# Performance work log

Hardware: AMD Instinct MI355X
Metric: run time of the kernel (lower is better)

The kernel has to match this reference:

```python
import jax, jax.numpy as jnp
import numpy as np

N_NODES = 50000
N_EDGES = 800000
F_IN = 32
H = 128
N_REL = 4
MAX_DEG = 10
N_GRAPHS = 64
N_BLOCKS = 2


def setup_inputs() -> dict:
    key = jax.random.key(0)
    ks = jax.random.split(key, 20)
    s = 0.05
    return {
        "x": jax.random.normal(ks[0], (N_NODES, F_IN), jnp.float32),
        "edge_index": jax.random.randint(ks[1], (2, N_EDGES), 0, N_NODES, dtype=jnp.int32),
        "edge_attr": jax.random.randint(ks[2], (N_EDGES,), 0, N_REL, dtype=jnp.int32),
        "batch_idx": jnp.sort(jax.random.randint(ks[3], (N_NODES,), 0, N_GRAPHS, dtype=jnp.int32)),
        "embed_W": jax.random.normal(ks[4], (F_IN, H), jnp.float32) * s,
        "embed_b": jax.random.normal(ks[5], (H,), jnp.float32) * s,
        "rgcn_Wrel": jax.random.normal(ks[6], (N_BLOCKS, N_REL, H, H), jnp.float32) * s,
        "rgcn_Wroot": jax.random.normal(ks[7], (N_BLOCKS, H, H), jnp.float32) * s,
        "rgcn_b": jax.random.normal(ks[8], (N_BLOCKS, H), jnp.float32) * s,
        "mf_Wl": jax.random.normal(ks[9], (N_BLOCKS, MAX_DEG + 1, H, H), jnp.float32) * s,
        "mf_bl": jax.random.normal(ks[10], (N_BLOCKS, MAX_DEG + 1, H), jnp.float32) * s,
        "mf_Wr": jax.random.normal(ks[11], (N_BLOCKS, MAX_DEG + 1, H, H), jnp.float32) * s,
        "lin1_W": jax.random.normal(ks[12], (H, H), jnp.float32) * s,
        "lin1_b": jax.random.normal(ks[13], (H,), jnp.float32) * s,
        "lin2_W": jax.random.normal(ks[14], (H, 1), jnp.float32) * s,
        "lin2_b": jax.random.normal(ks[15], (1,), jnp.float32) * s,
    }


def _rgcn(x, src, dst, rel, Wrel, Wroot, b):
    # PyG RGCNConv with default aggr='mean': per-relation mean over incoming
    # edges, then per-relation weight, plus root transform and bias.
    seg = dst * N_REL + rel  # composite segment id: (node, relation)
    agg = jax.ops.segment_sum(x[src], seg, num_segments=N_NODES * N_REL)
    cnt = jax.ops.segment_sum(jnp.ones((seg.shape[0],), x.dtype), seg,
                              num_segments=N_NODES * N_REL)
    agg = (agg / jnp.maximum(cnt, 1.0)[:, None]).reshape(N_NODES, N_REL, H)
    return jnp.einsum('nrh,rho->no', agg, Wrel) + x @ Wroot + b


def _mfconv(x, src, dst, Wl, bl, Wr):
    # PyG MFConv: sum-aggregate neighbors, then per-degree-bucket linear heads
    # (degree = in-degree clamped to MAX_DEG); lin_r applied to root x (no bias).
    h = jax.ops.segment_sum(x[src], dst, num_segments=N_NODES)  # [N,H]
    deg = jax.ops.segment_sum(jnp.ones((src.shape[0],), jnp.int32), dst,
                              num_segments=N_NODES)
    deg = jnp.minimum(deg, MAX_DEG)  # [N]
    # out_all: [D+1, N, H] candidate outputs, one per degree bucket
    out_all = (jnp.einsum('nh,dho->dno', h, Wl)
               + jnp.einsum('nh,dho->dno', x, Wr)
               + bl[:, None, :])
    return jnp.take_along_axis(out_all, deg[None, :, None], axis=0)[0]


def reference(x, edge_index, edge_attr, batch_idx, embed_W, embed_b,
              rgcn_Wrel, rgcn_Wroot, rgcn_b, mf_Wl, mf_bl, mf_Wr,
              lin1_W, lin1_b, lin2_W, lin2_b):
    src, dst = edge_index[0], edge_index[1]
    h = x @ embed_W + embed_b
    for blk in range(N_BLOCKS):
        if blk > 0:  # first block uses Identity instead of ReLU
            h = jax.nn.relu(h)
        h = _rgcn(h, src, dst, edge_attr, rgcn_Wrel[blk], rgcn_Wroot[blk], rgcn_b[blk])
        h = jax.nn.relu(h)
        h = _mfconv(h, src, dst, mf_Wl[blk], mf_bl[blk], mf_Wr[blk])
    g = jax.ops.segment_sum(h, batch_idx, num_segments=N_GRAPHS)  # global_add_pool
    g = jax.nn.relu(g @ lin1_W + lin1_b)
    return g @ lin2_W + lin2_b
```

## Files before the change

### kernel.cpp

```cpp
#include <hip/hip_runtime.h>
#include <hip/hip_bf16.h>

#define NRELS 4
#define MAXDEG 10
#define NBUCK 11
#define POOL_CHUNKS 8

typedef __attribute__((ext_vector_type(8))) short s16x8;
typedef __attribute__((ext_vector_type(4))) float f32x4;
typedef __attribute__((ext_vector_type(8))) unsigned short u16x8;

__device__ inline unsigned short f2b(float f) {
  __hip_bfloat16 h = __float2bfloat16(f);
  return *reinterpret_cast<unsigned short*>(&h);
}
__device__ inline float b2f(unsigned short u) {
  union { unsigned int i; float f; } v;
  v.i = ((unsigned int)u) << 16;
  return v.f;
}
__device__ inline float blo(unsigned int v) {
  union { unsigned int i; float f; } x;
  x.i = v << 16;
  return x.f;
}
__device__ inline float bhi(unsigned int v) {
  union { unsigned int i; float f; } x;
  x.i = v & 0xffff0000u;
  return x.f;
}

typedef __attribute__((address_space(3))) unsigned int lds_uint;
typedef __attribute__((address_space(1))) const unsigned int glob_uint;
__device__ __forceinline__ void gld_lds16(const void* g, void* l) {
  __builtin_amdgcn_global_load_lds((glob_uint*)g, (lds_uint*)l, 16, 0, 0);
}

__global__ __launch_bounds__(512) void coarse_count_scan(
    const int* __restrict__ dst, int* __restrict__ bhist, int* __restrict__ boff,
    int* __restrict__ bcur, int* __restrict__ done, int* __restrict__ perm, int permCap,
    int NB, int E, int nblocks) {
  __shared__ int lh[512];
  __shared__ int lastf;
  int t = threadIdx.x;
  lh[t] = 0;
  __syncthreads();
  for (int i = blockIdx.x * 512 + t; i < permCap; i += nblocks * 512) perm[i] = -1;
  int base = blockIdx.x * 4096;
  int lim = E - base;
  if (lim > 4096) lim = 4096;
  for (int i = t; i < lim; i += 512) atomicAdd(&lh[dst[base + i] >> 7], 1);
  __syncthreads();
  if (lh[t]) atomicAdd(&bhist[t], lh[t]);
  __threadfence();
  __syncthreads();
  if (t == 0) lastf = (atomicAdd(done, 1) == nblocks - 1) ? 1 : 0;
  __syncthreads();
  if (!lastf) return;
  int v = (t < NB) ? atomicAdd(&bhist[t], 0) : 0;
  lh[t] = v;
  __syncthreads();
  for (int o = 1; o < 512; o <<= 1) {
    int x = (t >= o) ? lh[t - o] : 0;
    __syncthreads();
    lh[t] += x;
    __syncthreads();
  }
  if (t < NB) {
    int st = lh[t] - v;
    boff[t] = st;
    bcur[t] = st;
  }
  if (t == 0) boff[NB] = E;
}

__global__ __launch_bounds__(512) void coarse_scatter(
    const int* __restrict__ src, const int* __restrict__ dst, const int* __restrict__ rel,
    int* __restrict__ bcur, uint2* __restrict__ ebuf, int E) {
  __shared__ int lhist[512];
  __shared__ int lstart[512];
  __shared__ int lcur[512];
  __shared__ int gbase[512];
  __shared__ uint2 stage[4096];
  int t = threadIdx.x;
  lhist[t] = 0;
  __syncthreads();
  int base = blockIdx.x * 4096;
  int lim = E - base;
  if (lim > 4096) lim = 4096;
  for (int i = t; i < lim; i += 512) atomicAdd(&lhist[dst[base + i] >> 7], 1);
  __syncthreads();
  int myc = lhist[t];
  lstart[t] = myc;
  __syncthreads();
  for (int o = 1; o < 512; o <<= 1) {
    int x = (t >= o) ? lstart[t - o] : 0;
    __syncthreads();
    lstart[t] += x;
    __syncthreads();
  }
  int incl = lstart[t];
  __syncthreads();
  lstart[t] = incl - myc;
  lcur[t] = 0;
  if (myc > 0) gbase[t] = atomicAdd(&bcur[t], myc);
  __syncthreads();
  for (int i = t; i < lim; i += 512) {
    int e = base + i;
    int d = dst[e];
    int b = d >> 7;
    int slot = lstart[b] + atomicAdd(&lcur[b], 1);
    stage[slot] = make_uint2((unsigned)(d * 4 + rel[e]), (unsigned)src[e]);
  }
  __syncthreads();
  for (int i = t; i < lim; i += 512) {
    uint2 val = stage[i];
    int b = (int)(val.x >> 9);
    ebuf[gbase[b] + (i - lstart[b])] = val;
  }
}

__global__ __launch_bounds__(512) void fine_place(
    const uint2* __restrict__ ebuf, const int* __restrict__ boff, int* __restrict__ cnt,
    int* __restrict__ seg_start, float* __restrict__ inv, int* __restrict__ deg,
    int* __restrict__ bucket, int* __restrict__ hist, int* __restrict__ csr, int NSEG) {
  __shared__ int lh[512];
  __shared__ int sc[512];
  __shared__ int lcur[512];
  __shared__ int lbh[16];
  int t = threadIdx.x;
  int b = blockIdx.x;
  lh[t] = 0;
  if (t < 16) lbh[t] = 0;
  __syncthreads();
  int s = boff[b], e = boff[b + 1];
  for (int i = s + t; i < e; i += 512) atomicAdd(&lh[ebuf[i].x & 511], 1);
  __syncthreads();
  int v = lh[t];
  sc[t] = v;
  __syncthreads();
  for (int o = 1; o < 512; o <<= 1) {
    int x = (t >= o) ? sc[t - o] : 0;
    __syncthreads();
    sc[t] += x;
    __syncthreads();
  }
  int gseg = b * 512 + t;
  int mystart = s + sc[t] - v;
  lcur[t] = mystart;
  if (gseg < NSEG) {
    cnt[gseg] = v;
    seg_start[gseg] = mystart;
    inv[gseg] = 1.0f / (float)(v > 1 ? v : 1);
    if ((t & 3) == 0) {
      int d = sc[t + 3] - sc[t] + v;
      int n = gseg >> 2;
      deg[n] = d;
      int bk = d < MAXDEG ? d : MAXDEG;
      bucket[n] = bk;
      atomicAdd(&lbh[bk], 1);
    }
  }
  __syncthreads();
  if (t < NBUCK && lbh[t]) atomicAdd(&hist[t], lbh[t]);
  for (int i = s + t; i < e; i += 512) {
    uint2 vv = ebuf[i];
    int pos = atomicAdd(&lcur[vv.x & 511], 1);
    csr[pos] = (int)vv.y;
  }
}

__global__ void build_perm(const int* __restrict__ bucket, const int* __restrict__ hist,
                           int* __restrict__ fill, int* __restrict__ perm, int N) {
  __shared__ int soff[NBUCK];
  __shared__ int lh[NBUCK];
  __shared__ int gbase[NBUCK];
  int t = threadIdx.x;
  if (t < NBUCK) lh[t] = 0;
  if (t == 0) {
    int acc = 0;
    for (int b = 0; b < NBUCK; b++) {
      soff[b] = acc;
      acc += ((hist[b] + 63) >> 6) << 6;
    }
  }
  __syncthreads();
  int n = blockIdx.x * 256 + t;
  int b = -1, lr = 0;
  if (n < N) {
    b = bucket[n];
    lr = atomicAdd(&lh[b], 1);
  }
  __syncthreads();
  if (t < NBUCK && lh[t] > 0) gbase[t] = atomicAdd(&fill[t * 16], lh[t]);
  __syncthreads();
  if (n < N) perm[soff[b] + gbase[b] + lr] = n;
}

__global__ __launch_bounds__(256) void embed_conv(
    const float* __restrict__ x, const float* __restrict__ embW,
    const float* __restrict__ bias, const float* __restrict__ Wrel,
    const float* __restrict__ Wroot, const float* __restrict__ Wl,
    const float* __restrict__ Wr, unsigned short* __restrict__ Bt,
    unsigned short* __restrict__ Btm, unsigned short* __restrict__ out, int N, int nbE) {
  if ((int)blockIdx.x >= nbE) {
    const int R1 = 2 * 128 * 640;
    const int R2 = R1 + 2 * 11 * 128 * 256;
    int t = (blockIdx.x - nbE) * 256 + threadIdx.x;
    if (t < R1) {
      int blk = t / 81920;
      int rem = t % 81920;
      int n = rem / 640;
      int k = rem % 640;
      float v;
      if (k < 512)
        v = Wrel[(size_t)blk * 65536 + (size_t)k * 128 + n];
      else
        v = Wroot[(size_t)blk * 16384 + (size_t)(k - 512) * 128 + n];
      Bt[t] = f2b(v);
    } else if (t < R2) {
      int t2 = t - R1;
      int k = t2 & 255;
      int n = (t2 >> 8) & 127;
      int bb = (t2 >> 15) % 11;
      int blk = t2 / (11 * 128 * 256);
      float v;
      if (k < 128)
        v = Wl[(((size_t)blk * 11 + bb) * 128 + k) * 128 + n];
      else
        v = Wr[(((size_t)blk * 11 + bb) * 128 + (k - 128)) * 128 + n];
      Btm[t2] = f2b(v);
    }
    return;
  }
  __shared__ unsigned char As[64 * 80];
  __shared__ unsigned char Bs[128 * 80];
  int t = threadIdx.x;
  int m0 = blockIdx.x * 64;
  {
    int r = t >> 2, s = t & 3;
    int gr = m0 + r;
    if (gr >= N) gr = N - 1;
    const float* xp = x + (size_t)gr * 32 + s * 8;
    float4 f0 = *(const float4*)xp;
    float4 f1 = *(const float4*)(xp + 4);
    u16x8 o;
    o[0] = f2b(f0.x); o[1] = f2b(f0.y); o[2] = f2b(f0.z); o[3] = f2b(f0.w);
    o[4] = f2b(f1.x); o[5] = f2b(f1.y); o[6] = f2b(f1.z); o[7] = f2b(f1.w);
    *(u16x8*)(As + r * 80 + s * 16) = o;
  }
  {
    int n = t >> 1, hf = t & 1;
    unsigned short tmp[16];
#pragma unroll
    for (int j = 0; j < 16; j++) tmp[j] = f2b(embW[(size_t)(hf * 16 + j) * 128 + n]);
    *(u16x8*)(Bs + n * 80 + hf * 32) = *(u16x8*)tmp;
    *(u16x8*)(Bs + n * 80 + hf * 32 + 16) = *(u16x8*)(tmp + 8);
  }
  __syncthreads();
  int lane = t & 63, wave = t >> 6;
  int row = lane & 15, quad = lane >> 4;
  int nh = wave * 32;
  f32x4 acc[2][4];
#pragma unroll
  for (int i = 0; i < 2; i++)
#pragma unroll
    for (int j = 0; j < 4; j++) acc[i][j] = (f32x4){0.f, 0.f, 0.f, 0.f};
  s16x8 af[4], bf[2];
#pragma unroll
  for (int mt = 0; mt < 4; mt++) {
    int R = mt * 16 + row;
    af[mt] = *(const s16x8*)(As + R * 80 + quad * 16);
  }
#pragma unroll
  for (int nt = 0; nt < 2; nt++) {
    int R = nh + nt * 16 + row;
    bf[nt] = *(const s16x8*)(Bs + R * 80 + quad * 16);
  }
#pragma unroll
  for (int nt = 0; nt < 2; nt++)
#pragma unroll
    for (int mt = 0; mt < 4; mt++)
      acc[nt][mt] = __builtin_amdgcn_mfma_f32_16x16x32_bf16(af[mt], bf[nt], acc[nt][mt], 0, 0, 0);
#pragma unroll
  for (int nt = 0; nt < 2; nt++) {
    int n = nh + nt * 16 + row;
    float bv = bias[n];
#pragma unroll
    for (int mt = 0; mt < 4; mt++) {
#pragma unroll
      for (int r4 = 0; r4 < 4; r4++) {
        int m = m0 + mt * 16 + quad * 4 + r4;
        if (m < N) out[(size_t)m * 128 + n] = f2b(acc[nt][mt][r4] + bv);
      }
    }
  }
}

__device__ __forceinline__ void acc8v(float* a, uint4 v) {
  a[0] += blo(v.x); a[1] += bhi(v.x);
  a[2] += blo(v.y); a[3] += bhi(v.y);
  a[4] += blo(v.z); a[5] += bhi(v.z);
  a[6] += blo(v.w); a[7] += bhi(v.w);
}

__device__ __forceinline__ void gather_seg(const unsigned short* __restrict__ hb,
                                           const int* __restrict__ csr, int st, int cn,
                                           int chunk, float* a) {
  const unsigned short* hq = hb + chunk * 16;
  int i = 0;
  for (; i + 2 <= cn; i += 2) {
    int p0 = csr[st + i], p1 = csr[st + i + 1];
    const uint4* r0 = (const uint4*)(hq + (size_t)p0 * 128);
    const uint4* r1 = (const uint4*)(hq + (size_t)p1 * 128);
    uint4 v00 = r0[0], v01 = r0[1];
    uint4 v10 = r1[0], v11 = r1[1];
    acc8v(a + 0, v00); acc8v(a + 8, v01);
    acc8v(a + 0, v10); acc8v(a + 8, v11);
  }
  if (i < cn) {
    const uint4* r0 = (const uint4*)(hq + (size_t)csr[st + i] * 128);
    acc8v(a + 0, r0[0]); acc8v(a + 8, r0[1]);
  }
}

__device__ __forceinline__ void gather2_seg(const unsigned short* __restrict__ hb,
                                            const int* __restrict__ csr,
                                            int st0, int cn0, int st1, int cn1,
                                            int chunk, float* a0, float* a1) {
  const unsigned short* hq = hb + chunk * 16;
  int mn = cn0 < cn1 ? cn0 : cn1;
  int i = 0;
  for (; i + 2 <= mn; i += 2) {
    int p00 = csr[st0 + i], p01 = csr[st0 + i + 1];
    int p10 = csr[st1 + i], p11 = csr[st1 + i + 1];
    const uint4* r00 = (const uint4*)(hq + (size_t)p00 * 128);
    const uint4* r01 = (const uint4*)(hq + (size_t)p01 * 128);
    const uint4* r10 = (const uint4*)(hq + (size_t)p10 * 128);
    const uint4* r11 = (const uint4*)(hq + (size_t)p11 * 128);
    uint4 v0a = r00[0], v0b = r00[1], v1a = r01[0], v1b = r01[1];
    uint4 v2a = r10[0], v2b = r10[1], v3a = r11[0], v3b = r11[1];
    acc8v(a0 + 0, v0a); acc8v(a0 + 8, v0b);
    acc8v(a0 + 0, v1a); acc8v(a0 + 8, v1b);
    acc8v(a1 + 0, v2a); acc8v(a1 + 8, v2b);
    acc8v(a1 + 0, v3a); acc8v(a1 + 8, v3b);
  }
  if (i < cn0) gather_seg(hb, csr, st0 + i, cn0 - i, chunk, a0);
  if (i < cn1) gather_seg(hb, csr, st1 + i, cn1 - i, chunk, a1);
}

__device__ __forceinline__ void write_frag(unsigned char* Ag, int ln, int chunk,
                                           const float* a, float w) {
  int s = chunk >> 2;
#pragma unroll
  for (int h = 0; h < 2; h++) {
    int c = (((chunk & 3) * 2 + h)) ^ (ln & 7);
    const float* p = a + h * 8;
    uint4 o;
    o.x = (unsigned int)f2b(p[0] * w) | ((unsigned int)f2b(p[1] * w) << 16);
    o.y = (unsigned int)f2b(p[2] * w) | ((unsigned int)f2b(p[3] * w) << 16);
    o.z = (unsigned int)f2b(p[4] * w) | ((unsigned int)f2b(p[5] * w) << 16);
    o.w = (unsigned int)f2b(p[6] * w) | ((unsigned int)f2b(p[7] * w) << 16);
    *(uint4*)(Ag + s * 8192 + ln * 128 + (c << 4)) = o;
  }
}

__device__ __forceinline__ void gemm_tile_gB(const unsigned char* Areg, const char* Bp,
                                             int strideB, int row, int quad, int nh,
                                             f32x4 acc[2][4]) {
#pragma unroll
  for (int s = 0; s < 2; s++) {
#pragma unroll
    for (int ks = 0; ks < 2; ks++) {
      int cch = ks * 4 + quad;
      s16x8 af[4], bf[2];
#pragma unroll
      for (int mt = 0; mt < 4; mt++) {
        int R = mt * 16 + row;
        af[mt] = *(const s16x8*)(Areg + s * 8192 + R * 128 + ((cch ^ (R & 7)) << 4));
      }
#pragma unroll
      for (int nt = 0; nt < 2; nt++) {
        int R = nh + nt * 16 + row;
        bf[nt] = *(const s16x8*)(Bp + (size_t)R * strideB + s * 128 + cch * 16);
      }
#pragma unroll
      for (int nt = 0; nt < 2; nt++)
#pragma unroll
        for (int mt = 0; mt < 4; mt++)
          acc[nt][mt] = __builtin_amdgcn_mfma_f32_16x16x32_bf16(af[mt], bf[nt], acc[nt][mt], 0, 0, 0);
    }
  }
}

__global__ __launch_bounds__(256) void rgcn_fused(
    const unsigned short* __restrict__ hb, const int* __restrict__ csr,
    const int* __restrict__ seg_start, const int* __restrict__ cnt,
    const float* __restrict__ inv, const int* __restrict__ perm,
    const unsigned short* __restrict__ Bt, const float* __restrict__ bias,
    unsigned short* __restrict__ out) {
  __shared__ unsigned char Ag[16384];
  __shared__ int nodes[64];
  int t = threadIdx.x;
  int m0 = blockIdx.x * 64;
  if (t < 64) nodes[t] = perm[m0 + t];
  __syncthreads();
  int lane = t & 63, wave = t >> 6;
  int row = lane & 15, quad = lane >> 4;
  int nh = wave * 32;
  int chunk = t & 7, lnb = t >> 3;
  int ln0 = lnb, ln1 = 32 + lnb;
  int nd0 = nodes[ln0], nd1 = nodes[ln1];
  f32x4 acc[2][4];
#pragma unroll
  for (int i = 0; i < 2; i++)
#pragma unroll
    for (int j = 0; j < 4; j++) acc[i][j] = (f32x4){0.f, 0.f, 0.f, 0.f};

  for (int rel = 0; rel < 4; rel++) {
    float a0[16], a1[16];
#pragma unroll
    for (int j = 0; j < 16; j++) { a0[j] = 0.f; a1[j] = 0.f; }
    int st0 = 0, cn0 = 0, st1 = 0, cn1 = 0;
    float w0 = 1.f, w1 = 1.f;
    if (nd0 >= 0) {
      int sid = nd0 * 4 + rel;
      st0 = seg_start[sid]; cn0 = cnt[sid]; w0 = inv[sid];
    }
    if (nd1 >= 0) {
      int sid = nd1 * 4 + rel;
      st1 = seg_start[sid]; cn1 = cnt[sid]; w1 = inv[sid];
    }
    gather2_seg(hb, csr, st0, cn0, st1, cn1, chunk, a0, a1);
    write_frag(Ag, ln0, chunk, a0, w0);
    write_frag(Ag, ln1, chunk, a1, w1);
    __syncthreads();
    gemm_tile_gB(Ag, (const char*)Bt + rel * 256, 1280, row, quad, nh, acc);
    __syncthreads();
  }
#pragma unroll
  for (int s = 0; s < 2; s++)
#pragma unroll
    for (int p = 0; p < 2; p++) {
      int o = s * 8192 + p * 4096 + t * 16;
      int r = (o >> 7) & 63, c = ((o >> 4) & 7) ^ (r & 7);
      int nd = nodes[r];
      if (nd < 0) nd = 0;
      gld_lds16((const char*)hb + (size_t)nd * 256 + s * 128 + c * 16, Ag + o);
    }
  __syncthreads();
  gemm_tile_gB(Ag, (const char*)Bt + 1024, 1280, row, quad, nh, acc);
#pragma unroll
  for (int nt = 0; nt < 2; nt++) {
    int n = nh + nt * 16 + row;
    float bv = bias[n];
#pragma unroll
    for (int mt = 0; mt < 4; mt++) {
#pragma unroll
      for (int r4 = 0; r4 < 4; r4++) {
        int nd = nodes[mt * 16 + quad * 4 + r4];
        if (nd >= 0) out[(size_t)nd * 128 + n] = f2b(fmaxf(acc[nt][mt][r4] + bv, 0.f));
      }
    }
  }
}

__global__ __launch_bounds__(256) void mf_fused(
    const unsigned short* __restrict__ hb, const int* __restrict__ csr,
    const int* __restrict__ seg_start, const int* __restrict__ deg,
    const int* __restrict__ perm, const int* __restrict__ hist,
    const unsigned short* __restrict__ Bt, const float* __restrict__ bl,
    unsigned short* __restrict__ out, int relu_out) {
  __shared__ unsigned char Ag[16384];
  __shared__ int nodes[64];
  __shared__ int soff[NBUCK + 1];
  int t = threadIdx.x;
  int m0 = blockIdx.x * 64;
  if (t == 0) {
    int a2 = 0;
    for (int b2 = 0; b2 < NBUCK; b2++) {
      soff[b2] = a2;
      a2 += ((hist[b2] + 63) >> 6) << 6;
    }
    soff[NBUCK] = a2;
  }
  if (t < 64) nodes[t] = perm[m0 + t];
  __syncthreads();
  if (m0 >= soff[NBUCK]) return;
  int b = 0;
  while (b < 10 && m0 >= soff[b + 1]) b++;
  const char* Bb = (const char*)(Bt + (size_t)b * 128 * 256);
  int lane = t & 63, wave = t >> 6;
  int row = lane & 15, quad = lane >> 4;
  int nh = wave * 32;
  int chunk = t & 7, lnb = t >> 3;
  int ln0 = lnb, ln1 = 32 + lnb;
  int nd0 = nodes[ln0], nd1 = nodes[ln1];
  f32x4 acc[2][4];
#pragma unroll
  for (int i = 0; i < 2; i++)
#pragma unroll
    for (int j = 0; j < 4; j++) acc[i][j] = (f32x4){0.f, 0.f, 0.f, 0.f};
  {
    float a0[16], a1[16];
#pragma unroll
    for (int j = 0; j < 16; j++) { a0[j] = 0.f; a1[j] = 0.f; }
    int st0 = 0, cn0 = 0, st1 = 0, cn1 = 0;
    if (nd0 >= 0) { st0 = seg_start[nd0 * 4]; cn0 = deg[nd0]; }
    if (nd1 >= 0) { st1 = seg_start[nd1 * 4]; cn1 = deg[nd1]; }
    gather2_seg(hb, csr, st0, cn0, st1, cn1, chunk, a0, a1);
    write_frag(Ag, ln0, chunk, a0, 1.f);
    write_frag(Ag, ln1, chunk, a1, 1.f);
  }
  __syncthreads();
  gemm_tile_gB(Ag, Bb, 512, row, quad, nh, acc);
  __syncthreads();
#pragma unroll
  for (int s = 0; s < 2; s++)
#pragma unroll
    for (int p = 0; p < 2; p++) {
      int o = s * 8192 + p * 4096 + t * 16;
      int r = (o >> 7) & 63, c = ((o >> 4) & 7) ^ (r & 7);
      int nd = nodes[r];
      if (nd < 0) nd = 0;
      gld_lds16((const char*)hb + (size_t)nd * 256 + s * 128 + c * 16, Ag + o);
    }
  __syncthreads();
  gemm_tile_gB(Ag, Bb + 256, 512, row, quad, nh, acc);
  const float* bb = bl + b * 128;
#pragma unroll
  for (int nt = 0; nt < 2; nt++) {
    int n = nh + nt * 16 + row;
    float bv = bb[n];
#pragma unroll
    for (int mt = 0; mt < 4; mt++) {
#pragma unroll
      for (int r4 = 0; r4 < 4; r4++) {
        int nd = nodes[mt * 16 + quad * 4 + r4];
        if (nd >= 0) {
          float v = acc[nt][mt][r4] + bv;
          if (relu_out) v = fmaxf(v, 0.f);
          out[(size_t)nd * 128 + n] = f2b(v);
        }
      }
    }
  }
}

__global__ void pool2(const unsigned short* __restrict__ h, const int* __restrict__ batch,
                      float* __restrict__ g, int N, int G) {
  int gr = blockIdx.x / POOL_CHUNKS;
  int ck = blockIdx.x % POOL_CHUNKS;
  int t = threadIdx.x;
  int lane = t & 63, grp = t >> 6;
  int lo = 0, hi = N;
  while (lo < hi) {
    int m = (lo + hi) >> 1;
    if (batch[m] < gr) lo = m + 1; else hi = m;
  }
  int s = lo;
  lo = s; hi = N;
  while (lo < hi) {
    int m = (lo + hi) >> 1;
    if (batch[m] < gr + 1) lo = m + 1; else hi = m;
  }
  int e = lo;
  int len = e - s;
  int a = s + (int)(((long long)len * ck) / POOL_CHUNKS);
  int b = s + (int)(((long long)len * (ck + 1)) / POOL_CHUNKS);
  float s0 = 0.f, s1 = 0.f;
  for (int n = a + grp; n < b; n += 2) {
    unsigned int v = *(const unsigned int*)(h + (size_t)n * 128 + lane * 2);
    s0 += blo(v);
    s1 += bhi(v);
  }
  if (b > a + grp) {
    atomicAdd(&g[gr * 128 + lane * 2], s0);
    atomicAdd(&g[gr * 128 + lane * 2 + 1], s1);
  }
}

__global__ void head_kernel(const float* __restrict__ g, const float* __restrict__ W1,
                            const float* __restrict__ b1, const float* __restrict__ W2,
                            const float* __restrict__ b2, float* __restrict__ out) {
  int bg = blockIdx.x;
  int o = threadIdx.x;
  __shared__ float gs[128];
  __shared__ float red[128];
  gs[o] = g[bg * 128 + o];
  __syncthreads();
  float acc = b1[o];
  for (int k = 0; k < 128; k++) acc += gs[k] * W1[k * 128 + o];
  acc = fmaxf(acc, 0.f);
  red[o] = acc * W2[o];
  __syncthreads();
  for (int s = 64; s > 0; s >>= 1) {
    if (o < s) red[o] += red[o + s];
    __syncthreads();
  }
  if (o == 0) out[bg] = red[0] + b2[0];
}

extern "C" void kernel_launch(void* const* d_in, const int* in_sizes, int n_in,
                              void* d_out, int out_size, void* d_ws, size_t ws_size,
                              hipStream_t stream) {
  const float* x = (const float*)d_in[0];
  const int* ei = (const int*)d_in[1];
  const int* ea = (const int*)d_in[2];
  const int* batch = (const int*)d_in[3];
  const float* embW = (const float*)d_in[4];
  const float* embB = (const float*)d_in[5];
  const float* Wrel = (const float*)d_in[6];
  const float* Wroot = (const float*)d_in[7];
  const float* rb = (const float*)d_in[8];
  const float* Wl = (const float*)d_in[9];
  const float* bl = (const float*)d_in[10];
  const float* Wr = (const float*)d_in[11];
  const float* l1W = (const float*)d_in[12];
  const float* l1b = (const float*)d_in[13];
  const float* l2W = (const float*)d_in[14];
  const float* l2b = (const float*)d_in[15];
  float* out = (float*)d_out;

  int N = in_sizes[0] / 32;
  int E = in_sizes[2];
  int G = out_size;
  int NSEG = N * 4;
  int NB = (N + 127) >> 7;

  char* p = (char*)d_ws;
  auto alloc = [&](size_t bytes) {
    char* r = p;
    p += (bytes + 255) & ~(size_t)255;
    return r;
  };
  int permCap = ((N + 63) / 64 + NBUCK) * 64;
  unsigned short* h_bf = (unsigned short*)alloc((size_t)N * 128 * 2);
  unsigned short* h2_bf = (unsigned short*)alloc((size_t)N * 128 * 2);
  unsigned short* Btr = (unsigned short*)alloc((size_t)2 * 128 * 640 * 2);
  unsigned short* Btm = (unsigned short*)alloc((size_t)2 * 11 * 128 * 256 * 2);
  float* inv = (float*)alloc((size_t)NSEG * 4);
  int* cnt = (int*)alloc((size_t)NSEG * 4);
  int* seg_start = (int*)alloc((size_t)NSEG * 4);
  int* csr = (int*)alloc((size_t)E * 4);
  uint2* ebuf = (uint2*)alloc((size_t)E * 8);
  int* deg = (int*)alloc((size_t)N * 4);
  int* bucket = (int*)alloc((size_t)N * 4);
  int* perm = (int*)alloc((size_t)permCap * 4);
  int* boff = (int*)alloc(516 * 4);
  int* bcur = (int*)alloc(512 * 4);
  size_t zeroBytes = 8192 + (size_t)G * 128 * 4;
  char* zb = alloc(zeroBytes);
  int* bhist = (int*)zb;
  int* hist = (int*)(zb + 4096);
  int* fill = (int*)(zb + 4608);
  int* done = (int*)(zb + 5376);
  float* g = (float*)(zb + 8192);

  (void)hipMemsetAsync(zb, 0, zeroBytes, stream);

  const int* src = ei;
  const int* dst = ei + E;

  int sblocks = (E + 4095) / 4096;
  coarse_count_scan<<<sblocks, 512, 0, stream>>>(dst, bhist, boff, bcur, done, perm, permCap,
                                                 NB, E, sblocks);
  coarse_scatter<<<sblocks, 512, 0, stream>>>(src, dst, ea, bcur, ebuf, E);
  fine_place<<<NB, 512, 0, stream>>>(ebuf, boff, cnt, seg_start, inv, deg, bucket, hist, csr,
                                     NSEG);
  build_perm<<<(N + 255) / 256, 256, 0, stream>>>(bucket, hist, fill, perm, N);

  int nbE = (N + 63) / 64;
  int convBlocks = (2 * 128 * 640 + 2 * 11 * 128 * 256 + 255) / 256;
  embed_conv<<<nbE + convBlocks, 256, 0, stream>>>(x, embW, embB, Wrel, Wroot, Wl, Wr, Btr,
                                                   Btm, h_bf, N, nbE);

  int mfblocks = permCap / 64;
  for (int blk = 0; blk < 2; blk++) {
    rgcn_fused<<<mfblocks, 256, 0, stream>>>(h_bf, csr, seg_start, cnt, inv, perm,
                                             Btr + (size_t)blk * 81920, rb + blk * 128,
                                             h2_bf);
    mf_fused<<<mfblocks, 256, 0, stream>>>(h2_bf, csr, seg_start, deg, perm, hist,
                                           Btm + (size_t)blk * 11 * 128 * 256,
                                           bl + (size_t)blk * 11 * 128, h_bf,
                                           (blk == 0) ? 1 : 0);
  }
  pool2<<<G * POOL_CHUNKS, 128, 0, stream>>>(h_bf, batch, g, N, G);
  head_kernel<<<G, 128, 0, stream>>>(g, l1W, l1b, l2W, l2b, out);
}
```

Before: 467.3 us.

## Double threads per block in fused RGCN/MF kernels, halving per-thread gather and GEMM work

The fused RGCN and MFConv kernels now launch 512 threads per 64-node tile instead of 256. Each thread gathers an 8-column (16-byte) slice of neighbor rows instead of 16 columns, and each wave computes a 16-wide output column strip instead of 32. The gather loop is unrolled by 4 to keep more independent loads in flight. This aims to raise memory-level parallelism and cut register pressure for the latency-bound neighbor gathers, at the cost of more waves reloading the A fragments from LDS and more threads sharing each barrier.

```diff
diff --git a/kernel.cpp b/kernel.cpp
--- a/kernel.cpp
+++ b/kernel.cpp
@@ -304,96 +304,71 @@
   a[6] += blo(v.w); a[7] += bhi(v.w);
 }
 
-__device__ __forceinline__ void gather_seg(const unsigned short* __restrict__ hb,
-                                           const int* __restrict__ csr, int st, int cn,
-                                           int chunk, float* a) {
-  const unsigned short* hq = hb + chunk * 16;
+__device__ __forceinline__ void gather_seg8(const unsigned short* __restrict__ hb,
+                                            const int* __restrict__ csr, int st, int cn,
+                                            int chunk, float* a) {
+  const unsigned short* hq = hb + chunk * 8;
   int i = 0;
-  for (; i + 2 <= cn; i += 2) {
+  for (; i + 4 <= cn; i += 4) {
     int p0 = csr[st + i], p1 = csr[st + i + 1];
-    const uint4* r0 = (const uint4*)(hq + (size_t)p0 * 128);
-    const uint4* r1 = (const uint4*)(hq + (size_t)p1 * 128);
-    uint4 v00 = r0[0], v01 = r0[1];
-    uint4 v10 = r1[0], v11 = r1[1];
-    acc8v(a + 0, v00); acc8v(a + 8, v01);
-    acc8v(a + 0, v10); acc8v(a + 8, v11);
+    int p2 = csr[st + i + 2], p3 = csr[st + i + 3];
+    uint4 v0 = *(const uint4*)(hq + (size_t)p0 * 128);
+    uint4 v1 = *(const uint4*)(hq + (size_t)p1 * 128);
+    uint4 v2 = *(const uint4*)(hq + (size_t)p2 * 128);
+    uint4 v3 = *(const uint4*)(hq + (size_t)p3 * 128);
+    acc8v(a, v0); acc8v(a, v1); acc8v(a, v2); acc8v(a, v3);
+  }
+  if (i + 2 <= cn) {
+    int p0 = csr[st + i], p1 = csr[st + i + 1];
+    uint4 v0 = *(const uint4*)(hq + (size_t)p0 * 128);
+    uint4 v1 = *(const uint4*)(hq + (size_t)p1 * 128);
+    acc8v(a, v0); acc8v(a, v1);
+    i += 2;
   }
   if (i < cn) {
-    const uint4* r0 = (const uint4*)(hq + (size_t)csr[st + i] * 128);
-    acc8v(a + 0, r0[0]); acc8v(a + 8, r0[1]);
-  }
-}
-
-__device__ __forceinline__ void gather2_seg(const unsigned short* __restrict__ hb,
-                                            const int* __restrict__ csr,
-                                            int st0, int cn0, int st1, int cn1,
-                                            int chunk, float* a0, float* a1) {
-  const unsigned short* hq = hb + chunk * 16;
-  int mn = cn0 < cn1 ? cn0 : cn1;
-  int i = 0;
-  for (; i + 2 <= mn; i += 2) {
-    int p00 = csr[st0 + i], p01 = csr[st0 + i + 1];
-    int p10 = csr[st1 + i], p11 = csr[st1 + i + 1];
-    const uint4* r00 = (const uint4*)(hq + (size_t)p00 * 128);
-    const uint4* r01 = (const uint4*)(hq + (size_t)p01 * 128);
-    const uint4* r10 = (const uint4*)(hq + (size_t)p10 * 128);
-    const uint4* r11 = (const uint4*)(hq + (size_t)p11 * 128);
-    uint4 v0a = r00[0], v0b = r00[1], v1a = r01[0], v1b = r01[1];
-    uint4 v2a = r10[0], v2b = r10[1], v3a = r11[0], v3b = r11[1];
-    acc8v(a0 + 0, v0a); acc8v(a0 + 8, v0b);
-    acc8v(a0 + 0, v1a); acc8v(a0 + 8, v1b);
-    acc8v(a1 + 0, v2a); acc8v(a1 + 8, v2b);
-    acc8v(a1 + 0, v3a); acc8v(a1 + 8, v3b);
-  }
-  if (i < cn0) gather_seg(hb, csr, st0 + i, cn0 - i, chunk, a0);
-  if (i < cn1) gather_seg(hb, csr, st1 + i, cn1 - i, chunk, a1);
-}
-
-__device__ __forceinline__ void write_frag(unsigned char* Ag, int ln, int chunk,
-                                           const float* a, float w) {
-  int s = chunk >> 2;
-#pragma unroll
-  for (int h = 0; h < 2; h++) {
-    int c = (((chunk & 3) * 2 + h)) ^ (ln & 7);
-    const float* p = a + h * 8;
-    uint4 o;
-    o.x = (unsigned int)f2b(p[0] * w) | ((unsigned int)f2b(p[1] * w) << 16);
-    o.y = (unsigned int)f2b(p[2] * w) | ((unsigned int)f2b(p[3] * w) << 16);
-    o.z = (unsigned int)f2b(p[4] * w) | ((unsigned int)f2b(p[5] * w) << 16);
-    o.w = (unsigned int)f2b(p[6] * w) | ((unsigned int)f2b(p[7] * w) << 16);
-    *(uint4*)(Ag + s * 8192 + ln * 128 + (c << 4)) = o;
-  }
-}
-
-__device__ __forceinline__ void gemm_tile_gB(const unsigned char* Areg, const char* Bp,
-                                             int strideB, int row, int quad, int nh,
-                                             f32x4 acc[2][4]) {
+    uint4 v0 = *(const uint4*)(hq + (size_t)csr[st + i] * 128);
+    acc8v(a, v0);
+  }
+}
+
+__device__ __forceinline__ void write_frag8(unsigned char* Ag, int ln, int chunk,
+                                            const float* a, float w) {
+  int s = chunk >> 3;
+  int c = (chunk & 7) ^ (ln & 7);
+  uint4 o;
+  o.x = (unsigned int)f2b(a[0] * w) | ((unsigned int)f2b(a[1] * w) << 16);
+  o.y = (unsigned int)f2b(a[2] * w) | ((unsigned int)f2b(a[3] * w) << 16);
+  o.z = (unsigned int)f2b(a[4] * w) | ((unsigned int)f2b(a[5] * w) << 16);
+  o.w = (unsigned int)f2b(a[6] * w) | ((unsigned int)f2b(a[7] * w) << 16);
+  *(uint4*)(Ag + s * 8192 + ln * 128 + (c << 4)) = o;
+}
+
+__device__ __forceinline__ void gemm_tile_gB8(const unsigned char* Areg, const char* Bp,
+                                              int strideB, int row, int quad, int nh,
+                                              f32x4 acc[4]) {
 #pragma unroll
   for (int s = 0; s < 2; s++) {
 #pragma unroll
     for (int ks = 0; ks < 2; ks++) {
       int cch = ks * 4 + quad;
-      s16x8 af[4], bf[2];
+      s16x8 af[4], bf;
 #pragma unroll
       for (int mt = 0; mt < 4; mt++) {
         int R = mt * 16 + row;
         af[mt] = *(const s16x8*)(Areg + s * 8192 + R * 128 + ((cch ^ (R & 7)) << 4));
       }
-#pragma unroll
-      for (int nt = 0; nt < 2; nt++) {
-        int R = nh + nt * 16 + row;
-        bf[nt] = *(const s16x8*)(Bp + (size_t)R * strideB + s * 128 + cch * 16);
+      {
+        int R = nh + row;
+        bf = *(const s16x8*)(Bp + (size_t)R * strideB + s * 128 + cch * 16);
       }
 #pragma unroll
-      for (int nt = 0; nt < 2; nt++)
-#pragma unroll
-        for (int mt = 0; mt < 4; mt++)
-          acc[nt][mt] = __builtin_amdgcn_mfma_f32_16x16x32_bf16(af[mt], bf[nt], acc[nt][mt], 0, 0, 0);
-    }
-  }
-}
-
-__global__ __launch_bounds__(256) void rgcn_fused(
+      for (int mt = 0; mt < 4; mt++)
+        acc[mt] = __builtin_amdgcn_mfma_f32_16x16x32_bf16(af[mt], bf, acc[mt], 0, 0, 0);
+    }
+  }
+}
+
+__global__ __launch_bounds__(512) void rgcn_fused(
     const unsigned short* __restrict__ hb, const int* __restrict__ csr,
     const int* __restrict__ seg_start, const int* __restrict__ cnt,
     const float* __restrict__ inv, const int* __restrict__ perm,
@@ -407,65 +382,68 @@
   __syncthreads();
   int lane = t & 63, wave = t >> 6;
   int row = lane & 15, quad = lane >> 4;
-  int nh = wave * 32;
-  int chunk = t & 7, lnb = t >> 3;
+  int nh = wave * 16;
+  int chunk = t & 15, lnb = t >> 4;
   int ln0 = lnb, ln1 = 32 + lnb;
   int nd0 = nodes[ln0], nd1 = nodes[ln1];
-  f32x4 acc[2][4];
-#pragma unroll
-  for (int i = 0; i < 2; i++)
-#pragma unroll
-    for (int j = 0; j < 4; j++) acc[i][j] = (f32x4){0.f, 0.f, 0.f, 0.f};
+  f32x4 acc[4];
+#pragma unroll
+  for (int j = 0; j < 4; j++) acc[j] = (f32x4){0.f, 0.f, 0.f, 0.f};
 
   for (int rel = 0; rel < 4; rel++) {
-    float a0[16], a1[16];
-#pragma unroll
-    for (int j = 0; j < 16; j++) { a0[j] = 0.f; a1[j] = 0.f; }
-    int st0 = 0, cn0 = 0, st1 = 0, cn1 = 0;
-    float w0 = 1.f, w1 = 1.f;
-    if (nd0 >= 0) {
-      int sid = nd0 * 4 + rel;
-      st0 = seg_start[sid]; cn0 = cnt[sid]; w0 = inv[sid];
-    }
-    if (nd1 >= 0) {
-      int sid = nd1 * 4 + rel;
-      st1 = seg_start[sid]; cn1 = cnt[sid]; w1 = inv[sid];
-    }
-    gather2_seg(hb, csr, st0, cn0, st1, cn1, chunk, a0, a1);
-    write_frag(Ag, ln0, chunk, a0, w0);
-    write_frag(Ag, ln1, chunk, a1, w1);
-    __syncthreads();
-    gemm_tile_gB(Ag, (const char*)Bt + rel * 256, 1280, row, quad, nh, acc);
-    __syncthreads();
-  }
-#pragma unroll
-  for (int s = 0; s < 2; s++)
-#pragma unroll
-    for (int p = 0; p < 2; p++) {
-      int o = s * 8192 + p * 4096 + t * 16;
-      int r = (o >> 7) & 63, c = ((o >> 4) & 7) ^ (r & 7);
-      int nd = nodes[r];
-      if (nd < 0) nd = 0;
-      gld_lds16((const char*)hb + (size_t)nd * 256 + s * 128 + c * 16, Ag + o);
-    }
-  __syncthreads();
-  gemm_tile_gB(Ag, (const char*)Bt + 1024, 1280, row, quad, nh, acc);
-#pragma unroll
-  for (int nt = 0; nt < 2; nt++) {
-    int n = nh + nt * 16 + row;
+    {
+      float a0[8];
+#pragma unroll
+      for (int j = 0; j < 8; j++) a0[j] = 0.f;
+      float w0 = 1.f;
+      if (nd0 >= 0) {
+        int sid = nd0 * 4 + rel;
+        w0 = inv[sid];
+        gather_seg8(hb, csr, seg_start[sid], cnt[sid], chunk, a0);
+      }
+      write_frag8(Ag, ln0, chunk, a0, w0);
+    }
+    {
+      float a1[8];
+#pragma unroll
+      for (int j = 0; j < 8; j++) a1[j] = 0.f;
+      float w1 = 1.f;
+      if (nd1 >= 0) {
+        int sid = nd1 * 4 + rel;
+        w1 = inv[sid];
+        gather_seg8(hb, csr, seg_start[sid], cnt[sid], chunk, a1);
+      }
+      write_frag8(Ag, ln1, chunk, a1, w1);
+    }
+    __syncthreads();
+    gemm_tile_gB8(Ag, (const char*)Bt + rel * 256, 1280, row, quad, nh, acc);
+    __syncthreads();
+  }
+#pragma unroll
+  for (int s = 0; s < 2; s++) {
+    int o = s * 8192 + t * 16;
+    int r = (o >> 7) & 63, c = ((o >> 4) & 7) ^ (r & 7);
+    int nd = nodes[r];
+    if (nd < 0) nd = 0;
+    gld_lds16((const char*)hb + (size_t)nd * 256 + s * 128 + c * 16, Ag + o);
+  }
+  __syncthreads();
+  gemm_tile_gB8(Ag, (const char*)Bt + 1024, 1280, row, quad, nh, acc);
+  {
+    int n = nh + row;
     float bv = bias[n];
 #pragma unroll
     for (int mt = 0; mt < 4; mt++) {
 #pragma unroll
       for (int r4 = 0; r4 < 4; r4++) {
         int nd = nodes[mt * 16 + quad * 4 + r4];
-        if (nd >= 0) out[(size_t)nd * 128 + n] = f2b(fmaxf(acc[nt][mt][r4] + bv, 0.f));
+        if (nd >= 0) out[(size_t)nd * 128 + n] = f2b(fmaxf(acc[mt][r4] + bv, 0.f));
       }
     }
   }
 }
 
-__global__ __launch_bounds__(256) void mf_fused(
+__global__ __launch_bounds__(512) void mf_fused(
     const unsigned short* __restrict__ hb, const int* __restrict__ csr,
     const int* __restrict__ seg_start, const int* __restrict__ deg,
     const int* __restrict__ perm, const int* __restrict__ hist,
@@ -492,45 +470,43 @@
   const char* Bb = (const char*)(Bt + (size_t)b * 128 * 256);
   int lane = t & 63, wave = t >> 6;
   int row = lane & 15, quad = lane >> 4;
-  int nh = wave * 32;
-  int chunk = t & 7, lnb = t >> 3;
+  int nh = wave * 16;
+  int chunk = t & 15, lnb = t >> 4;
   int ln0 = lnb, ln1 = 32 + lnb;
   int nd0 = nodes[ln0], nd1 = nodes[ln1];
-  f32x4 acc[2][4];
-#pragma unroll
-  for (int i = 0; i < 2; i++)
-#pragma unroll
-    for (int j = 0; j < 4; j++) acc[i][j] = (f32x4){0.f, 0.f, 0.f, 0.f};
+  f32x4 acc[4];
+#pragma unroll
+  for (int j = 0; j < 4; j++) acc[j] = (f32x4){0.f, 0.f, 0.f, 0.f};
   {
-    float a0[16], a1[16];
-#pragma unroll
-    for (int j = 0; j < 16; j++) { a0[j] = 0.f; a1[j] = 0.f; }
-    int st0 = 0, cn0 = 0, st1 = 0, cn1 = 0;
-    if (nd0 >= 0) { st0 = seg_start[nd0 * 4]; cn0 = deg[nd0]; }
-    if (nd1 >= 0) { st1 = seg_start[nd1 * 4]; cn1 = deg[nd1]; }
-    gather2_seg(hb, csr, st0, cn0, st1, cn1, chunk, a0, a1);
-    write_frag(Ag, ln0, chunk, a0, 1.f);
-    write_frag(Ag, ln1, chunk, a1, 1.f);
-  }
-  __syncthreads();
-  gemm_tile_gB(Ag, Bb, 512, row, quad, nh, acc);
-  __syncthreads();
-#pragma unroll
-  for (int s = 0; s < 2; s++)
-#pragma unroll
-    for (int p = 0; p < 2; p++) {
-      int o = s * 8192 + p * 4096 + t * 16;
-      int r = (o >> 7) & 63, c = ((o >> 4) & 7) ^ (r & 7);
-      int nd = nodes[r];
-      if (nd < 0) nd = 0;
-      gld_lds16((const char*)hb + (size_t)nd * 256 + s * 128 + c * 16, Ag + o);
-    }
-  __syncthreads();
-  gemm_tile_gB(Ag, Bb + 256, 512, row, quad, nh, acc);
+    float a0[8];
+#pragma unroll
+    for (int j = 0; j < 8; j++) a0[j] = 0.f;
+    if (nd0 >= 0) gather_seg8(hb, csr, seg_start[nd0 * 4], deg[nd0], chunk, a0);
+    write_frag8(Ag, ln0, chunk, a0, 1.f);
+  }
+  {
+    float a1[8];
+#pragma unroll
+    for (int j = 0; j < 8; j++) a1[j] = 0.f;
+    if (nd1 >= 0) gather_seg8(hb, csr, seg_start[nd1 * 4], deg[nd1], chunk, a1);
+    write_frag8(Ag, ln1, chunk, a1, 1.f);
+  }
+  __syncthreads();
+  gemm_tile_gB8(Ag, Bb, 512, row, quad, nh, acc);
+  __syncthreads();
+#pragma unroll
+  for (int s = 0; s < 2; s++) {
+    int o = s * 8192 + t * 16;
+    int r = (o >> 7) & 63, c = ((o >> 4) & 7) ^ (r & 7);
+    int nd = nodes[r];
+    if (nd < 0) nd = 0;
+    gld_lds16((const char*)hb + (size_t)nd * 256 + s * 128 + c * 16, Ag + o);
+  }
+  __syncthreads();
+  gemm_tile_gB8(Ag, Bb + 256, 512, row, quad, nh, acc);
   const float* bb = bl + b * 128;
-#pragma unroll
-  for (int nt = 0; nt < 2; nt++) {
-    int n = nh + nt * 16 + row;
+  {
+    int n = nh + row;
     float bv = bb[n];
 #pragma unroll
     for (int mt = 0; mt < 4; mt++) {
@@ -538,7 +514,7 @@
       for (int r4 = 0; r4 < 4; r4++) {
         int nd = nodes[mt * 16 + quad * 4 + r4];
         if (nd >= 0) {
-          float v = acc[nt][mt][r4] + bv;
+          float v = acc[mt][r4] + bv;
           if (relu_out) v = fmaxf(v, 0.f);
           out[(size_t)nd * 128 + n] = f2b(v);
         }
@@ -677,10 +653,10 @@
 
   int mfblocks = permCap / 64;
   for (int blk = 0; blk < 2; blk++) {
-    rgcn_fused<<<mfblocks, 256, 0, stream>>>(h_bf, csr, seg_start, cnt, inv, perm,
+    rgcn_fused<<<mfblocks, 512, 0, stream>>>(h_bf, csr, seg_start, cnt, inv, perm,
                                              Btr + (size_t)blk * 81920, rb + blk * 128,
                                              h2_bf);
-    mf_fused<<<mfblocks, 256, 0, stream>>>(h2_bf, csr, seg_start, deg, perm, hist,
+    mf_fused<<<mfblocks, 512, 0, stream>>>(h2_bf, csr, seg_start, deg, perm, hist,
                                            Btm + (size_t)blk * 11 * 128 * 256,
                                            bl + (size_t)blk * 11 * 128, h_bf,
                                            (blk == 0) ? 1 : 0);
```

Result: faster. 409.9 us (-12.3%).
